# Kernel optimization log

Measured on AMD Instinct MI355X. Metric: run time of the kernel, lower is better.

Reference implementation:

```python
import jax, jax.numpy as jnp
import numpy as np

HID = 1024
H = 8        # num_attention_heads
KV = 2       # num_key_value_heads
HD = HID // H  # head_dim = 128
G = H // KV    # kv groups = 4
EPS = 1e-6


def setup_inputs() -> dict:
    key = jax.random.key(0)
    ks = jax.random.split(key, 12)
    B, S = 4, 2048
    s = 0.02
    inp = {
        "hidden_states": jax.random.normal(ks[0], (B, S, HID), jnp.float32),
        "rope": jax.random.normal(ks[1], (1, 1, S, 2 * HD), jnp.float32),
        # q_proj outputs 2*H*HD (query + elementwise gate)
        "Wq": jax.random.normal(ks[2], (HID, 2 * H * HD), jnp.float32) * s,
        "bq": jnp.zeros((2 * H * HD,), jnp.float32),
        "Wk": jax.random.normal(ks[3], (HID, KV * HD), jnp.float32) * s,
        "bk": jnp.zeros((KV * HD,), jnp.float32),
        "Wv": jax.random.normal(ks[4], (HID, KV * HD), jnp.float32) * s,
        "bv": jnp.zeros((KV * HD,), jnp.float32),
        "Wo": jax.random.normal(ks[5], (H * HD, HID), jnp.float32) * s,
        "bo": jnp.zeros((HID,), jnp.float32),
        "q_norm_w": jnp.ones((HD,), jnp.float32),
        "k_norm_w": jnp.ones((HD,), jnp.float32),
    }
    return inp


def _rmsnorm(x, w):
    var = jnp.mean(jnp.square(x), axis=-1, keepdims=True)
    return x * jax.lax.rsqrt(var + EPS) * w


def _rot(x):
    # interleaved rotation: [-x1, x0, -x3, x2, ...]
    x2 = x.reshape(x.shape[:-1] + (HD // 2, 2))
    r = jnp.stack([-x2[..., 1], x2[..., 0]], axis=-1)
    return r.reshape(x.shape)


def _apply_rope_cat(x, emb):
    # emb: [S, 2*HD] = cat(sin, cos); x: [B, h, S, HD]
    sin, cos = jnp.split(emb, 2, axis=-1)
    sin = sin[None, None]
    cos = cos[None, None]
    return x * cos + _rot(x) * sin


def reference(hidden_states, rope, Wq, bq, Wk, bk, Wv, bv, Wo, bo, q_norm_w, k_norm_w):
    B, S, _ = hidden_states.shape
    qg = hidden_states @ Wq + bq                     # [B,S,2*H*HD]
    qg = qg.reshape(B, S, KV, -1)                    # [B,S,KV, 2*G*HD]
    q, gate = jnp.split(qg, [HD * G], axis=-1)       # [B,S,KV,G*HD], [B,S,KV,G*HD]
    gate = gate.reshape(B, S, H, HD)                 # [B,S,H,HD]
    q = q.reshape(B, S, H, HD).transpose(0, 2, 1, 3) # [B,H,S,HD]
    k = (hidden_states @ Wk + bk).reshape(B, S, KV, HD).transpose(0, 2, 1, 3)
    v = (hidden_states @ Wv + bv).reshape(B, S, KV, HD).transpose(0, 2, 1, 3)

    q = _rmsnorm(q, q_norm_w)
    k = _rmsnorm(k, k_norm_w)

    emb = rope[0, 0, :S]                             # [S, 2*HD]
    q = _apply_rope_cat(q, emb)
    k = _apply_rope_cat(k, emb)

    # GQA: repeat kv heads to match query heads
    k = jnp.repeat(k, G, axis=1)                     # [B,H,S,HD]
    v = jnp.repeat(v, G, axis=1)

    scale = 1.0 / jnp.sqrt(jnp.asarray(HD, q.dtype))
    scores = jnp.einsum("bhqd,bhkd->bhqk", q, k) * scale
    attn = jax.nn.softmax(scores, axis=-1)
    out = jnp.einsum("bhqk,bhkd->bhqd", attn, v)     # [B,H,S,HD]

    out = out.transpose(0, 2, 1, 3)                  # [B,S,H,HD]
    out = out * jax.nn.sigmoid(gate)
    out = out.reshape(B, S, H * HD)
    return out @ Wo + bo
```

## Files before the change

### kernel.cpp

```cpp
#include <hip/hip_runtime.h>
#include <math.h>

#define SCALE_ 0.08838834764831845f
#define PSHIFT 8.0f

typedef __attribute__((ext_vector_type(8))) short short8;
typedef __attribute__((ext_vector_type(4))) float floatx4;
typedef __attribute__((ext_vector_type(4))) _Float16 half4;
typedef __attribute__((ext_vector_type(8))) _Float16 half8;

__device__ inline short f2bf(float x) {
    union { float f; unsigned u; } v; v.f = x;
    unsigned r = v.u + 0x7fff + ((v.u >> 16) & 1);
    return (short)(r >> 16);
}
__device__ inline float bf2f(short h) {
    union { float f; unsigned u; } v; v.u = ((unsigned)(unsigned short)h) << 16;
    return v.f;
}

__global__ __launch_bounds__(256) void prep_fused(
    const float* __restrict__ X, short* __restrict__ Xb,
    const float* __restrict__ bq, const float* __restrict__ bk2,
    const float* __restrict__ bv2, float* __restrict__ bcat,
    const float* __restrict__ Wq, const float* __restrict__ Wk,
    const float* __restrict__ Wv, const float* __restrict__ Wo,
    short* __restrict__ Wt, short* __restrict__ Wot)
{
    __shared__ float T[32][33];
    const int bid = blockIdx.x;
    const int t = threadIdx.x;
    if (bid < 8192) {
        const int gid = bid * 256 + t;
        if (gid < 2097152) {
            const float4 v = ((const float4*)X)[gid];
            short4 o;
            o.x = f2bf(v.x); o.y = f2bf(v.y); o.z = f2bf(v.z); o.w = f2bf(v.w);
            ((short4*)Xb)[gid] = o;
        }
        if (gid < 2560)
            bcat[gid] = (gid < 2048) ? bq[gid]
                      : (gid < 2304) ? bk2[gid - 2048] : bv2[gid - 2304];
        return;
    }
    const int t2 = bid - 8192;
    const int k0 = (t2 & 31) * 32;
    const int ny = t2 >> 5;
    const float* src; int ldn, ncol0, nrow0; short* dst;
    if (ny < 80) {
        const int n0 = ny * 32;
        if (n0 < 2048)      { src = Wq; ldn = 2048; ncol0 = n0; }
        else if (n0 < 2304) { src = Wk; ldn = 256;  ncol0 = n0 - 2048; }
        else                { src = Wv; ldn = 256;  ncol0 = n0 - 2304; }
        dst = Wt; nrow0 = n0;
    } else {
        const int n0 = (ny - 80) * 32;
        src = Wo; ldn = 1024; ncol0 = n0; dst = Wot; nrow0 = n0;
    }
    {
        const int r = t >> 3, c4 = (t & 7) * 4;
        const float4 v = *(const float4*)&src[(size_t)(k0 + r) * ldn + ncol0 + c4];
        T[r][c4 + 0] = v.x; T[r][c4 + 1] = v.y; T[r][c4 + 2] = v.z; T[r][c4 + 3] = v.w;
    }
    __syncthreads();
    {
        const int nr = t >> 3, kc4 = (t & 7) * 4;
        short4 o;
        o.x = f2bf(T[kc4 + 0][nr]);
        o.y = f2bf(T[kc4 + 1][nr]);
        o.z = f2bf(T[kc4 + 2][nr]);
        o.w = f2bf(T[kc4 + 3][nr]);
        *(short4*)&dst[(size_t)(nrow0 + nr) * 1024 + k0 + kc4] = o;
    }
}

__global__ __launch_bounds__(256) void qkv_mfma(
    const short* __restrict__ Ag, const short* __restrict__ Bg,
    const float* __restrict__ bcat,
    const float* __restrict__ rope,
    const float* __restrict__ qw, const float* __restrict__ kw,
    short* __restrict__ qb, short* __restrict__ kb,
    _Float16* __restrict__ vt, short* __restrict__ gateb)
{
    __shared__ short As[128 * 64];
    __shared__ short Bs[128 * 64];
    __shared__ _Float16 vscr[128 * 68];
    __shared__ float sred[256];
    const int tid = threadIdx.x;
    const int wave = tid >> 6, lane = tid & 63;
    const int quad = lane >> 4, l16 = lane & 15;
    const int wm = wave & 1, wn = wave >> 1;
    const int lin = blockIdx.x;
    const int xcd = lin & 7;
    const int idx = lin >> 3;
    const int rr_ = idx / 20;
    const int m0 = (xcd * 8 + rr_) * 128;
    const int n0 = (idx - rr_ * 20) * 128;

    floatx4 acc[4][4] = {};

    for (int k0 = 0; k0 < 1024; k0 += 64) {
        __syncthreads();
        #pragma unroll
        for (int c = 0; c < 4; ++c) {
            const int blk = (c * 4 + wave) * 64 + lane;
            const int row = blk >> 3, p = blk & 7;
            const int col = (p ^ (row & 7)) << 3;
            __builtin_amdgcn_global_load_lds(
                (const __attribute__((address_space(1))) unsigned int*)(Ag + (size_t)(m0 + row) * 1024 + k0 + col),
                (__attribute__((address_space(3))) unsigned int*)&As[(c * 4 + wave) * 512],
                16, 0, 0);
            __builtin_amdgcn_global_load_lds(
                (const __attribute__((address_space(1))) unsigned int*)(Bg + (size_t)(n0 + row) * 1024 + k0 + col),
                (__attribute__((address_space(3))) unsigned int*)&Bs[(c * 4 + wave) * 512],
                16, 0, 0);
        }
        __syncthreads();
        #pragma unroll
        for (int ks = 0; ks < 2; ++ks) {
            short8 af[4], bfr[4];
            #pragma unroll
            for (int mt = 0; mt < 4; ++mt) {
                const int row = wm * 64 + mt * 16 + l16;
                const int p = (ks * 4 + quad) ^ (row & 7);
                af[mt] = *(const short8*)&As[row * 64 + p * 8];
            }
            #pragma unroll
            for (int nt = 0; nt < 4; ++nt) {
                const int row = wn * 64 + nt * 16 + l16;
                const int p = (ks * 4 + quad) ^ (row & 7);
                bfr[nt] = *(const short8*)&Bs[row * 64 + p * 8];
            }
            #pragma unroll
            for (int mt = 0; mt < 4; ++mt)
                #pragma unroll
                for (int nt = 0; nt < 4; ++nt)
                    acc[mt][nt] = __builtin_amdgcn_mfma_f32_16x16x32_bf16(af[mt], bfr[nt], acc[mt][nt], 0, 0, 0);
        }
    }

    const int dl0 = wn * 64 + l16;
    float bias4[4];
    #pragma unroll
    for (int nt = 0; nt < 4; ++nt) bias4[nt] = bcat[n0 + dl0 + nt * 16];
    const int nlow = n0 & 1023;

    if (n0 >= 2304) {
        const int kvv = (n0 - 2304) >> 7;
        const int bV = m0 >> 11, s0g = m0 & 2047;
        const size_t vtb = ((size_t)(bV * 2 + kvv)) * 128 * 2048;
        __syncthreads();
        #pragma unroll
        for (int half = 0; half < 2; ++half) {
            if (wn == half) {
                #pragma unroll
                for (int mt = 0; mt < 4; ++mt)
                    #pragma unroll
                    for (int r = 0; r < 4; ++r) {
                        const int sl = wm * 64 + mt * 16 + quad * 4 + r;
                        #pragma unroll
                        for (int nt = 0; nt < 4; ++nt)
                            vscr[sl * 68 + nt * 16 + l16] =
                                (_Float16)(acc[mt][nt][r] + bias4[nt]);
                    }
            }
            __syncthreads();
            {
                const int dl = tid & 63, sch = tid >> 6;
                #pragma unroll
                for (int g = 0; g < 8; ++g) {
                    half4 o;
                    #pragma unroll
                    for (int e = 0; e < 4; ++e)
                        o[e] = vscr[(sch * 32 + g * 4 + e) * 68 + dl];
                    const int ncs = (g < 4) ? (g << 1) : (((g - 4) << 1) | 1);
                    *(half4*)&vt[vtb + (size_t)(half * 64 + dl) * 2048 + s0g + sch * 32 + ncs * 4] = o;
                }
            }
            __syncthreads();
        }
    } else if (n0 < 2048 && nlow >= 512) {
        const int h = ((n0 >> 10) << 2) + ((nlow - 512) >> 7);
        #pragma unroll
        for (int nt = 0; nt < 4; ++nt) {
            const int d = dl0 + nt * 16;
            #pragma unroll
            for (int mt = 0; mt < 4; ++mt)
                #pragma unroll
                for (int r = 0; r < 4; ++r) {
                    const int m = m0 + wm * 64 + mt * 16 + quad * 4 + r;
                    gateb[(size_t)m * 1024 + h * 128 + d] = f2bf(acc[mt][nt][r] + bias4[nt]);
                }
        }
    } else {
        const int isQ = (n0 < 2048);
        const int hq  = isQ ? (((n0 >> 10) << 2) + (nlow >> 7)) : 0;
        const int kvk = isQ ? 0 : ((n0 - 2048) >> 7);
        const float* wv = isQ ? qw : kw;
        const float scl = isQ ? SCALE_ : 1.0f;
        short* dst = isQ ? qb : kb;

        __syncthreads();
        float part[4][4];
        #pragma unroll
        for (int mt = 0; mt < 4; ++mt)
            #pragma unroll
            for (int r = 0; r < 4; ++r) {
                float p = 0.f;
                #pragma unroll
                for (int nt = 0; nt < 4; ++nt) {
                    const float x = acc[mt][nt][r] + bias4[nt];
                    p += x * x;
                }
                #pragma unroll
                for (int off = 1; off < 16; off <<= 1)
                    p += __shfl_xor(p, off);
                part[mt][r] = p;
            }
        if (wn == 1 && l16 == 0) {
            #pragma unroll
            for (int mt = 0; mt < 4; ++mt)
                #pragma unroll
                for (int r = 0; r < 4; ++r)
                    sred[wm * 64 + mt * 16 + quad * 4 + r] = part[mt][r];
        }
        __syncthreads();
        if (wn == 0 && l16 == 0) {
            #pragma unroll
            for (int mt = 0; mt < 4; ++mt)
                #pragma unroll
                for (int r = 0; r < 4; ++r) {
                    const int ml = wm * 64 + mt * 16 + quad * 4 + r;
                    const float tot = part[mt][r] + sred[ml];
                    sred[128 + ml] = rsqrtf(tot * (1.0f / 128.0f) + 1e-6f);
                }
        }
        __syncthreads();
        float w4[4];
        #pragma unroll
        for (int nt = 0; nt < 4; ++nt) w4[nt] = wv[dl0 + nt * 16];
        #pragma unroll
        for (int mt = 0; mt < 4; ++mt)
            #pragma unroll
            for (int r = 0; r < 4; ++r) {
                const int m = m0 + wm * 64 + mt * 16 + quad * 4 + r;
                const int bb = m >> 11, s = m & 2047;
                const float inv = sred[128 + wm * 64 + mt * 16 + quad * 4 + r];
                const float* er = rope + (size_t)s * 256;
                const size_t rb = ((size_t)(isQ ? (bb * 8 + hq) : (bb * 2 + kvk)) * 2048 + s) * 128;
                #pragma unroll
                for (int nt = 0; nt < 4; ++nt) {
                    const int d = dl0 + nt * 16;
                    const float xn = (acc[mt][nt][r] + bias4[nt]) * inv * w4[nt];
                    const float pn = __shfl_xor(xn, 1);
                    const float sn = er[d], cn = er[128 + d];
                    const float out = (l16 & 1) ? fmaf(xn, cn, pn * sn)
                                                : fmaf(xn, cn, -pn * sn);
                    dst[rb + d] = f2bf(out * scl);
                }
            }
    }
}

__global__ __launch_bounds__(256, 2) void attn_mfma(
    const short* __restrict__ qb, const short* __restrict__ kb,
    const _Float16* __restrict__ vt, const short* __restrict__ gateb,
    short* __restrict__ xo)
{
    __shared__ short    Ks[2][64 * 128];
    __shared__ _Float16 VTs[2][128 * 64];

    const int tid = threadIdx.x;
    const int wave = tid >> 6, lane = tid & 63;
    const int quad = lane >> 4, l16 = lane & 15;
    const int bh = blockIdx.y, b = bh >> 3, h = bh & 7, kv = h >> 2;
    const int q0 = blockIdx.x * 128;

    short8 qf[4][2];
    #pragma unroll
    for (int u = 0; u < 2; ++u) {
        const short* qbase = qb + (((size_t)(b * 8 + h)) * 2048 + q0 + wave * 32 + u * 16 + l16) * 128;
        #pragma unroll
        for (int ks = 0; ks < 4; ++ks)
            qf[ks][u] = *(const short8*)&qbase[ks * 32 + quad * 8];
    }

    const short*    kbase  = kb + (size_t)(b * 2 + kv) * 2048 * 128;
    const _Float16* vtbase = vt + (size_t)(b * 2 + kv) * 128 * 2048;

    int koff[4], voff[4];
    #pragma unroll
    for (int c = 0; c < 4; ++c) {
        const int sidx = (c * 4 + wave) * 64 + lane;
        { const int r = sidx >> 4, p = sidx & 15;
          koff[c] = r * 128 + ((p ^ (r & 7)) << 3); }
        { const int r = sidx >> 3, p = sidx & 7;
          voff[c] = r * 2048 + ((p ^ (r & 7)) << 3); }
    }

    floatx4 O[8][2] = {};
    float lsum[2] = {0.0f, 0.0f};

    #pragma unroll
    for (int c = 0; c < 4; ++c) {
        __builtin_amdgcn_global_load_lds(
            (const __attribute__((address_space(1))) unsigned int*)(kbase + koff[c]),
            (__attribute__((address_space(3))) unsigned int*)&Ks[0][(c * 4 + wave) * 512],
            16, 0, 0);
        __builtin_amdgcn_global_load_lds(
            (const __attribute__((address_space(1))) unsigned int*)(vtbase + voff[c]),
            (__attribute__((address_space(3))) unsigned int*)&VTs[0][(c * 4 + wave) * 512],
            16, 0, 0);
    }

    for (int kt = 0; kt < 32; ++kt) {
        const int cur = kt & 1;
        __syncthreads();

        if (kt + 1 < 32) {
            const short*    kg = kbase  + (size_t)(kt + 1) * 8192;
            const _Float16* vg = vtbase + (kt + 1) * 64;
            #pragma unroll
            for (int c = 0; c < 4; ++c) {
                __builtin_amdgcn_global_load_lds(
                    (const __attribute__((address_space(1))) unsigned int*)(kg + koff[c]),
                    (__attribute__((address_space(3))) unsigned int*)&Ks[cur ^ 1][(c * 4 + wave) * 512],
                    16, 0, 0);
                __builtin_amdgcn_global_load_lds(
                    (const __attribute__((address_space(1))) unsigned int*)(vg + voff[c]),
                    (__attribute__((address_space(3))) unsigned int*)&VTs[cur ^ 1][(c * 4 + wave) * 512],
                    16, 0, 0);
            }
        }

        #pragma unroll
        for (int t = 0; t < 2; ++t) {
            floatx4 ST[2][2];
            #pragma unroll
            for (int j = 0; j < 2; ++j) {
                ST[j][0] = (floatx4){0.f, 0.f, 0.f, 0.f};
                ST[j][1] = (floatx4){0.f, 0.f, 0.f, 0.f};
                const int krow = (2 * t + j) * 16 + l16;
                #pragma unroll
                for (int ks = 0; ks < 4; ++ks) {
                    const short8 af = *(const short8*)&Ks[cur][krow * 128 + (((ks * 4 + quad) ^ (l16 & 7)) << 3)];
                    ST[j][0] = __builtin_amdgcn_mfma_f32_16x16x32_bf16(af, qf[ks][0], ST[j][0], 0, 0, 0);
                    ST[j][1] = __builtin_amdgcn_mfma_f32_16x16x32_bf16(af, qf[ks][1], ST[j][1], 0, 0, 0);
                }
            }

            half8 pf[2];
            #pragma unroll
            for (int u = 0; u < 2; ++u) {
                #pragma unroll
                for (int r = 0; r < 4; ++r) {
                    const float plo = __expf(ST[0][u][r] - PSHIFT);
                    const float phi = __expf(ST[1][u][r] - PSHIFT);
                    lsum[u] += plo + phi;
                    pf[u][r]     = (_Float16)plo;
                    pf[u][4 + r] = (_Float16)phi;
                }
            }

            #pragma unroll
            for (int dt = 0; dt < 8; ++dt) {
                const half8 va = *(const half8*)&VTs[cur][(dt * 16 + l16) * 64 + (((4 * t + quad) ^ (l16 & 7)) << 3)];
                O[dt][0] = __builtin_amdgcn_mfma_f32_16x16x32_f16(va, pf[0], O[dt][0], 0, 0, 0);
                O[dt][1] = __builtin_amdgcn_mfma_f32_16x16x32_f16(va, pf[1], O[dt][1], 0, 0, 0);
            }
        }
    }

    #pragma unroll
    for (int u = 0; u < 2; ++u) {
        float ps = lsum[u];
        ps += __shfl_xor(ps, 16);
        ps += __shfl_xor(ps, 32);
        const float invl = 1.0f / ps;
        const int s = q0 + wave * 32 + u * 16 + l16;
        const size_t base = ((size_t)b * 2048 + s) * 1024 + h * 128;
        #pragma unroll
        for (int dt = 0; dt < 8; ++dt) {
            const int d0 = dt * 16 + quad * 4;
            const short4 g4 = *(const short4*)&gateb[base + d0];
            short4 o4;
            o4.x = f2bf(O[dt][u][0] * invl * (1.0f / (1.0f + __expf(-bf2f(g4.x)))));
            o4.y = f2bf(O[dt][u][1] * invl * (1.0f / (1.0f + __expf(-bf2f(g4.y)))));
            o4.z = f2bf(O[dt][u][2] * invl * (1.0f / (1.0f + __expf(-bf2f(g4.z)))));
            o4.w = f2bf(O[dt][u][3] * invl * (1.0f / (1.0f + __expf(-bf2f(g4.w)))));
            *(short4*)&xo[base + d0] = o4;
        }
    }
}

__global__ __launch_bounds__(256) void out_mfma(
    const short* __restrict__ Ag, const short* __restrict__ Bg,
    const float* __restrict__ bo, float* __restrict__ Y)
{
    __shared__ short As[128 * 64];
    __shared__ short Bs[128 * 64];
    const int tid = threadIdx.x;
    const int wave = tid >> 6, lane = tid & 63;
    const int quad = lane >> 4, l16 = lane & 15;
    const int wm = wave & 1, wn = wave >> 1;
    const int lin = blockIdx.x;
    const int xcd = lin & 7;
    const int idx = lin >> 3;
    const int m0 = (xcd * 8 + (idx >> 3)) * 128;
    const int n0 = (idx & 7) * 128;

    floatx4 acc[4][4] = {};

    for (int k0 = 0; k0 < 1024; k0 += 64) {
        __syncthreads();
        #pragma unroll
        for (int c = 0; c < 4; ++c) {
            const int blk = (c * 4 + wave) * 64 + lane;
            const int row = blk >> 3, p = blk & 7;
            const int col = (p ^ (row & 7)) << 3;
            __builtin_amdgcn_global_load_lds(
                (const __attribute__((address_space(1))) unsigned int*)(Ag + (size_t)(m0 + row) * 1024 + k0 + col),
                (__attribute__((address_space(3))) unsigned int*)&As[(c * 4 + wave) * 512],
                16, 0, 0);
            __builtin_amdgcn_global_load_lds(
                (const __attribute__((address_space(1))) unsigned int*)(Bg + (size_t)(n0 + row) * 1024 + k0 + col),
                (__attribute__((address_space(3))) unsigned int*)&Bs[(c * 4 + wave) * 512],
                16, 0, 0);
        }
        __syncthreads();
        #pragma unroll
        for (int ks = 0; ks < 2; ++ks) {
            short8 af[4], bfr[4];
            #pragma unroll
            for (int mt = 0; mt < 4; ++mt) {
                const int row = wm * 64 + mt * 16 + l16;
                const int p = (ks * 4 + quad) ^ (row & 7);
                af[mt] = *(const short8*)&As[row * 64 + p * 8];
            }
            #pragma unroll
            for (int nt = 0; nt < 4; ++nt) {
                const int row = wn * 64 + nt * 16 + l16;
                const int p = (ks * 4 + quad) ^ (row & 7);
                bfr[nt] = *(const short8*)&Bs[row * 64 + p * 8];
            }
            #pragma unroll
            for (int mt = 0; mt < 4; ++mt)
                #pragma unroll
                for (int nt = 0; nt < 4; ++nt)
                    acc[mt][nt] = __builtin_amdgcn_mfma_f32_16x16x32_bf16(af[mt], bfr[nt], acc[mt][nt], 0, 0, 0);
        }
    }

    #pragma unroll
    for (int nt = 0; nt < 4; ++nt) {
        const int n = n0 + wn * 64 + nt * 16 + l16;
        const float bias = bo[n];
        #pragma unroll
        for (int mt = 0; mt < 4; ++mt) {
            #pragma unroll
            for (int r = 0; r < 4; ++r) {
                const int m = m0 + wm * 64 + mt * 16 + quad * 4 + r;
                Y[(size_t)m * 1024 + n] = acc[mt][nt][r] + bias;
            }
        }
    }
}

extern "C" void kernel_launch(void* const* d_in, const int* in_sizes, int n_in,
                              void* d_out, int out_size, void* d_ws, size_t ws_size,
                              hipStream_t stream) {
    (void)in_sizes; (void)n_in; (void)out_size; (void)ws_size;
    const float* hs   = (const float*)d_in[0];
    const float* rope = (const float*)d_in[1];
    const float* Wq   = (const float*)d_in[2];
    const float* bq   = (const float*)d_in[3];
    const float* Wk   = (const float*)d_in[4];
    const float* bk   = (const float*)d_in[5];
    const float* Wv   = (const float*)d_in[6];
    const float* bv   = (const float*)d_in[7];
    const float* Wo   = (const float*)d_in[8];
    const float* bo   = (const float*)d_in[9];
    const float* qw   = (const float*)d_in[10];
    const float* kw   = (const float*)d_in[11];
    float* out = (float*)d_out;

    short* qb    = (short*)d_ws;
    short* kbuf  = qb    + (size_t)8388608;
    short* vb    = kbuf  + (size_t)2097152;
    _Float16* vt = (_Float16*)(vb + (size_t)2097152);
    short* gateb = (short*)(vt + (size_t)2097152);
    short* xb    = gateb + (size_t)8388608;
    short* wt    = xb    + (size_t)8388608;
    short* wot   = wt    + (size_t)2621440;
    float* bcat  = (float*)(wot + (size_t)1048576);

    prep_fused<<<dim3(11776), 256, 0, stream>>>(hs, xb, bq, bk, bv, bcat,
                                                Wq, Wk, Wv, Wo, wt, wot);
    qkv_mfma<<<dim3(1280), 256, 0, stream>>>(xb, wt, bcat, rope, qw, kw,
                                             qb, kbuf, vt, gateb);
    attn_mfma<<<dim3(16, 32), 256, 0, stream>>>(qb, kbuf, vt, gateb, xb);
    out_mfma<<<dim3(512), 256, 0, stream>>>(xb, wot, bo, out);
}
```

Measured before the change: 283.8 us.

## Split attention KV tile across wave pairs and reduce partial outputs in LDS

The attention block now covers 64 queries instead of 128. Each pair of waves handles half of every 64-key tile (split-K within the block), and partial O accumulators and row sums are combined through shared memory at the end. The grid doubles to 1024 blocks, which gives more parallelism across CUs. In exchange, each K/V tile loaded into LDS is reused by half as many queries, so global traffic rises, and there is an extra LDS reduction plus a larger shared allocation (about 65KB) that may limit occupancy.

```diff
diff --git a/kernel.cpp b/kernel.cpp
--- a/kernel.cpp
+++ b/kernel.cpp
@@ -267,19 +267,23 @@
     const _Float16* __restrict__ vt, const short* __restrict__ gateb,
     short* __restrict__ xo)
 {
-    __shared__ short    Ks[2][64 * 128];
-    __shared__ _Float16 VTs[2][128 * 64];
+    __shared__ __align__(16) char smem[66560];
+    short*    Ks   = (short*)smem;
+    _Float16* VTs  = (_Float16*)(smem + 32768);
+    floatx4*  comb = (floatx4*)smem;
+    float*    Lred = (float*)(smem + 65536);
 
     const int tid = threadIdx.x;
     const int wave = tid >> 6, lane = tid & 63;
     const int quad = lane >> 4, l16 = lane & 15;
+    const int qg = wave & 1, kh = wave >> 1;
     const int bh = blockIdx.y, b = bh >> 3, h = bh & 7, kv = h >> 2;
-    const int q0 = blockIdx.x * 128;
+    const int q0 = blockIdx.x * 64;
 
     short8 qf[4][2];
     #pragma unroll
     for (int u = 0; u < 2; ++u) {
-        const short* qbase = qb + (((size_t)(b * 8 + h)) * 2048 + q0 + wave * 32 + u * 16 + l16) * 128;
+        const short* qbase = qb + (((size_t)(b * 8 + h)) * 2048 + q0 + qg * 32 + u * 16 + l16) * 128;
         #pragma unroll
         for (int ks = 0; ks < 4; ++ks)
             qf[ks][u] = *(const short8*)&qbase[ks * 32 + quad * 8];
@@ -305,11 +309,11 @@
     for (int c = 0; c < 4; ++c) {
         __builtin_amdgcn_global_load_lds(
             (const __attribute__((address_space(1))) unsigned int*)(kbase + koff[c]),
-            (__attribute__((address_space(3))) unsigned int*)&Ks[0][(c * 4 + wave) * 512],
+            (__attribute__((address_space(3))) unsigned int*)&Ks[(c * 4 + wave) * 512],
             16, 0, 0);
         __builtin_amdgcn_global_load_lds(
             (const __attribute__((address_space(1))) unsigned int*)(vtbase + voff[c]),
-            (__attribute__((address_space(3))) unsigned int*)&VTs[0][(c * 4 + wave) * 512],
+            (__attribute__((address_space(3))) unsigned int*)&VTs[(c * 4 + wave) * 512],
             16, 0, 0);
     }
 
@@ -324,71 +328,82 @@
             for (int c = 0; c < 4; ++c) {
                 __builtin_amdgcn_global_load_lds(
                     (const __attribute__((address_space(1))) unsigned int*)(kg + koff[c]),
-                    (__attribute__((address_space(3))) unsigned int*)&Ks[cur ^ 1][(c * 4 + wave) * 512],
+                    (__attribute__((address_space(3))) unsigned int*)&Ks[(cur ^ 1) * 8192 + (c * 4 + wave) * 512],
                     16, 0, 0);
                 __builtin_amdgcn_global_load_lds(
                     (const __attribute__((address_space(1))) unsigned int*)(vg + voff[c]),
-                    (__attribute__((address_space(3))) unsigned int*)&VTs[cur ^ 1][(c * 4 + wave) * 512],
+                    (__attribute__((address_space(3))) unsigned int*)&VTs[(cur ^ 1) * 8192 + (c * 4 + wave) * 512],
                     16, 0, 0);
             }
         }
 
-        #pragma unroll
-        for (int t = 0; t < 2; ++t) {
-            floatx4 ST[2][2];
-            #pragma unroll
-            for (int j = 0; j < 2; ++j) {
-                ST[j][0] = (floatx4){0.f, 0.f, 0.f, 0.f};
-                ST[j][1] = (floatx4){0.f, 0.f, 0.f, 0.f};
-                const int krow = (2 * t + j) * 16 + l16;
-                #pragma unroll
-                for (int ks = 0; ks < 4; ++ks) {
-                    const short8 af = *(const short8*)&Ks[cur][krow * 128 + (((ks * 4 + quad) ^ (l16 & 7)) << 3)];
-                    ST[j][0] = __builtin_amdgcn_mfma_f32_16x16x32_bf16(af, qf[ks][0], ST[j][0], 0, 0, 0);
-                    ST[j][1] = __builtin_amdgcn_mfma_f32_16x16x32_bf16(af, qf[ks][1], ST[j][1], 0, 0, 0);
-                }
-            }
-
-            half8 pf[2];
-            #pragma unroll
-            for (int u = 0; u < 2; ++u) {
-                #pragma unroll
-                for (int r = 0; r < 4; ++r) {
-                    const float plo = __expf(ST[0][u][r] - PSHIFT);
-                    const float phi = __expf(ST[1][u][r] - PSHIFT);
-                    lsum[u] += plo + phi;
-                    pf[u][r]     = (_Float16)plo;
-                    pf[u][4 + r] = (_Float16)phi;
-                }
-            }
-
+        floatx4 ST[2][2];
+        #pragma unroll
+        for (int j = 0; j < 2; ++j) {
+            ST[j][0] = (floatx4){0.f, 0.f, 0.f, 0.f};
+            ST[j][1] = (floatx4){0.f, 0.f, 0.f, 0.f};
+            const int krow = kh * 32 + j * 16 + l16;
+            #pragma unroll
+            for (int ks = 0; ks < 4; ++ks) {
+                const short8 af = *(const short8*)&Ks[cur * 8192 + krow * 128 + (((ks * 4 + quad) ^ (l16 & 7)) << 3)];
+                ST[j][0] = __builtin_amdgcn_mfma_f32_16x16x32_bf16(af, qf[ks][0], ST[j][0], 0, 0, 0);
+                ST[j][1] = __builtin_amdgcn_mfma_f32_16x16x32_bf16(af, qf[ks][1], ST[j][1], 0, 0, 0);
+            }
+        }
+
+        half8 pf[2];
+        #pragma unroll
+        for (int u = 0; u < 2; ++u) {
+            #pragma unroll
+            for (int r = 0; r < 4; ++r) {
+                const float plo = __expf(ST[0][u][r] - PSHIFT);
+                const float phi = __expf(ST[1][u][r] - PSHIFT);
+                lsum[u] += plo + phi;
+                pf[u][r]     = (_Float16)plo;
+                pf[u][4 + r] = (_Float16)phi;
+            }
+        }
+
+        #pragma unroll
+        for (int dt = 0; dt < 8; ++dt) {
+            const half8 va = *(const half8*)&VTs[cur * 8192 + (dt * 16 + l16) * 64 + (((4 * kh + quad) ^ (l16 & 7)) << 3)];
+            O[dt][0] = __builtin_amdgcn_mfma_f32_16x16x32_f16(va, pf[0], O[dt][0], 0, 0, 0);
+            O[dt][1] = __builtin_amdgcn_mfma_f32_16x16x32_f16(va, pf[1], O[dt][1], 0, 0, 0);
+        }
+    }
+
+    __syncthreads();
+    if (kh == 1) {
+        #pragma unroll
+        for (int u = 0; u < 2; ++u) {
+            Lred[(qg * 2 + u) * 64 + lane] = lsum[u];
+            #pragma unroll
+            for (int dt = 0; dt < 8; ++dt)
+                comb[((qg * 2 + u) * 8 + dt) * 64 + lane] = O[dt][u];
+        }
+    }
+    __syncthreads();
+    if (kh == 0) {
+        #pragma unroll
+        for (int u = 0; u < 2; ++u) {
+            float ps = lsum[u] + Lred[(qg * 2 + u) * 64 + lane];
+            ps += __shfl_xor(ps, 16);
+            ps += __shfl_xor(ps, 32);
+            const float invl = 1.0f / ps;
+            const int s = q0 + qg * 32 + u * 16 + l16;
+            const size_t base = ((size_t)b * 2048 + s) * 1024 + h * 128;
             #pragma unroll
             for (int dt = 0; dt < 8; ++dt) {
-                const half8 va = *(const half8*)&VTs[cur][(dt * 16 + l16) * 64 + (((4 * t + quad) ^ (l16 & 7)) << 3)];
-                O[dt][0] = __builtin_amdgcn_mfma_f32_16x16x32_f16(va, pf[0], O[dt][0], 0, 0, 0);
-                O[dt][1] = __builtin_amdgcn_mfma_f32_16x16x32_f16(va, pf[1], O[dt][1], 0, 0, 0);
-            }
-        }
-    }
-
-    #pragma unroll
-    for (int u = 0; u < 2; ++u) {
-        float ps = lsum[u];
-        ps += __shfl_xor(ps, 16);
-        ps += __shfl_xor(ps, 32);
-        const float invl = 1.0f / ps;
-        const int s = q0 + wave * 32 + u * 16 + l16;
-        const size_t base = ((size_t)b * 2048 + s) * 1024 + h * 128;
-        #pragma unroll
-        for (int dt = 0; dt < 8; ++dt) {
-            const int d0 = dt * 16 + quad * 4;
-            const short4 g4 = *(const short4*)&gateb[base + d0];
-            short4 o4;
-            o4.x = f2bf(O[dt][u][0] * invl * (1.0f / (1.0f + __expf(-bf2f(g4.x)))));
-            o4.y = f2bf(O[dt][u][1] * invl * (1.0f / (1.0f + __expf(-bf2f(g4.y)))));
-            o4.z = f2bf(O[dt][u][2] * invl * (1.0f / (1.0f + __expf(-bf2f(g4.z)))));
-            o4.w = f2bf(O[dt][u][3] * invl * (1.0f / (1.0f + __expf(-bf2f(g4.w)))));
-            *(short4*)&xo[base + d0] = o4;
+                const floatx4 oc = O[dt][u] + comb[((qg * 2 + u) * 8 + dt) * 64 + lane];
+                const int d0 = dt * 16 + quad * 4;
+                const short4 g4 = *(const short4*)&gateb[base + d0];
+                short4 o4;
+                o4.x = f2bf(oc[0] * invl * (1.0f / (1.0f + __expf(-bf2f(g4.x)))));
+                o4.y = f2bf(oc[1] * invl * (1.0f / (1.0f + __expf(-bf2f(g4.y)))));
+                o4.z = f2bf(oc[2] * invl * (1.0f / (1.0f + __expf(-bf2f(g4.z)))));
+                o4.w = f2bf(oc[3] * invl * (1.0f / (1.0f + __expf(-bf2f(g4.w)))));
+                *(short4*)&xo[base + d0] = o4;
+            }
         }
     }
 }
@@ -498,6 +513,6 @@
                                                 Wq, Wk, Wv, Wo, wt, wot);
     qkv_mfma<<<dim3(1280), 256, 0, stream>>>(xb, wt, bcat, rope, qw, kw,
                                              qb, kbuf, vt, gateb);
-    attn_mfma<<<dim3(16, 32), 256, 0, stream>>>(qb, kbuf, vt, gateb, xb);
+    attn_mfma<<<dim3(32, 32), 256, 0, stream>>>(qb, kbuf, vt, gateb, xb);
     out_mfma<<<dim3(512), 256, 0, stream>>>(xb, wot, bo, out);
 }
```

Result: slower. 290.3 us (+2.3%).
